# Performance work log

Measured on AMD Instinct MI355X. Metric: run time of the kernel, lower is better.

The kernel has to match this reference:

```python
import jax, jax.numpy as jnp
import numpy as np
from jax import lax

V = 50000      # node_num
LN = 128       # feat_dim
S = 16         # stat_dim
E = 500000     # n_edges
T = 3          # propagation steps
MU = 0.9


def setup_inputs() -> dict:
    key = jax.random.key(0)
    ks = jax.random.split(key, 10)
    X_Node = jax.random.randint(ks[0], (E,), 0, V, dtype=jnp.int32)
    X_Neis = jax.random.randint(ks[1], (E,), 0, V, dtype=jnp.int32)
    dg_list = jax.random.randint(ks[2], (E,), 1, 64, dtype=jnp.int32)
    emb = jax.random.normal(ks[3], (V, LN), dtype=jnp.float32) * 0.1
    xi_w = jax.random.normal(ks[4], (2 * LN, S * S), dtype=jnp.float32) * (1.0 / np.sqrt(2 * LN))
    xi_b = jnp.zeros((S * S,), dtype=jnp.float32)
    rou_w = jax.random.normal(ks[5], (LN, S), dtype=jnp.float32) * (1.0 / np.sqrt(LN))
    rou_b = jnp.zeros((S,), dtype=jnp.float32)
    lin_w = jax.random.normal(ks[6], (LN + S, 3), dtype=jnp.float32) * (1.0 / np.sqrt(LN + S))
    lin_b = jnp.zeros((3,), dtype=jnp.float32)
    return {"X_Node": X_Node, "X_Neis": X_Neis, "dg_list": dg_list,
            "emb": emb, "xi_w": xi_w, "xi_b": xi_b,
            "rou_w": rou_w, "rou_b": rou_b, "lin_w": lin_w, "lin_b": lin_b}


def reference(X_Node, X_Neis, dg_list, emb, xi_w, xi_b, rou_w, rou_b, lin_w, lin_b):
    # edge features: concat(src embed, nbr embed) -> [E, 2*ln]
    Xn = emb[X_Node]                                  # [E, ln]
    X = jnp.concatenate([Xn, emb[X_Neis]], axis=1)    # [E, 2*ln]
    dg = dg_list.astype(emb.dtype)
    # Hw: A = Xi(X)*mu/s/dg  (constant across iterations; torch recomputes, same math)
    A = jnp.tanh(X @ xi_w + xi_b).reshape(-1, S, S)   # [E, s, s]
    A = A * (MU / S) / dg[:, None, None]
    b = jnp.tanh(Xn @ rou_w + rou_b)                  # [E, s]

    states0 = jnp.zeros((V, S), dtype=emb.dtype)

    def step(states, _):
        H = states[X_Node]                            # [E, s] gather
        H = jnp.einsum('est,et->es', A, H) + b        # per-edge small matvec
        states = jax.ops.segment_sum(H, X_Neis, num_segments=V)  # scatter-sum (AggrSum)
        return states, None

    states, _ = lax.scan(step, states0, None, length=T)
    logits = jnp.concatenate([emb, states], axis=1) @ lin_w + lin_b  # [V, 3]
    return jax.nn.softmax(logits, axis=1)
```

## Files before the change

### kernel.cpp

```cpp
#include <hip/hip_runtime.h>
#include <hip/hip_bf16.h>
#include <hip/hip_fp16.h>

#define LN_F 128

typedef __attribute__((ext_vector_type(8))) __bf16 bf16x8;
typedef __attribute__((ext_vector_type(4))) float f32x4;

__device__ __forceinline__ unsigned short f2bf(float f) {
    unsigned u = __float_as_uint(f);
    u = u + 0x7FFFu + ((u >> 16) & 1u);
    return (unsigned short)(u >> 16);
}
__device__ __forceinline__ unsigned cvt_pk_bf16(float lo, float hi) {
    unsigned r;
    asm("v_cvt_pk_bf16_f32 %0, %1, %2" : "=v"(r) : "v"(lo), "v"(hi));
    return r;
}
__device__ __forceinline__ float tanh_poly(float x) {
    float t = x * x;
    float p = fmaf(t, -0.05396825397f, 0.13333333333f);
    p = fmaf(t, p, -0.33333333333f);
    p = fmaf(t, p, 1.0f);
    return x * p;
}
__device__ __forceinline__ float tanh_polyc(float x) {
    return tanh_poly(fminf(1.2f, fmaxf(-1.2f, x)));
}
__device__ __forceinline__ float bflo(unsigned u) { return __uint_as_float(u << 16); }
__device__ __forceinline__ float bfhi(unsigned u) { return __uint_as_float(u & 0xffff0000u); }

__device__ __forceinline__ unsigned f2e5(float x) {
    unsigned short u = __half_as_ushort(__float2half(x));
    u = (unsigned short)(u + 0x7F + ((u >> 8) & 1));
    return (unsigned)(u >> 8) & 0xFFu;
}
__device__ __forceinline__ float2 cvt2f16(unsigned w) {
    union { unsigned u; __half2 h; } cv;
    cv.u = w;
    return __half22float2(cv.h);
}

__global__ void k_conv_emb(const float* __restrict__ src,
                           unsigned short* __restrict__ dst, int n8) {
    int i = blockIdx.x * blockDim.x + threadIdx.x;
    if (i >= n8) return;
    const float4* s = (const float4*)src;
    float4 a = s[i * 2], b = s[i * 2 + 1];
    uint4 o;
    o.x = (unsigned)f2bf(a.x) | ((unsigned)f2bf(a.y) << 16);
    o.y = (unsigned)f2bf(a.z) | ((unsigned)f2bf(a.w) << 16);
    o.z = (unsigned)f2bf(b.x) | ((unsigned)f2bf(b.y) << 16);
    o.w = (unsigned)f2bf(b.z) | ((unsigned)f2bf(b.w) << 16);
    ((uint4*)dst)[i] = o;
}

__global__ void k_conv_wc(const float* __restrict__ xiw, unsigned short* __restrict__ dst) {
    int t = blockIdx.x * blockDim.x + threadIdx.x;
    if (t >= 512 * 16) return;
    int cp = t >> 4, g = t & 15;
    unsigned short u[8];
#pragma unroll
    for (int j = 0; j < 8; ++j) {
        int k = g * 8 + j;
        float w = (cp < 256) ? xiw[k * 256 + cp] : xiw[(128 + k) * 256 + (cp - 256)];
        u[j] = f2bf(w);
    }
    uint4 o;
    o.x = (unsigned)u[0] | ((unsigned)u[1] << 16);
    o.y = (unsigned)u[2] | ((unsigned)u[3] << 16);
    o.z = (unsigned)u[4] | ((unsigned)u[5] << 16);
    o.w = (unsigned)u[6] | ((unsigned)u[7] << 16);
    ((uint4*)dst)[cp * 16 + (g ^ (cp & 7))] = o;
}

__global__ void k_conv_rou(const float* __restrict__ w, unsigned short* __restrict__ dst) {
    int t = blockIdx.x * blockDim.x + threadIdx.x;
    if (t >= 16 * 16) return;
    int c = t >> 4, g = t & 15;
    unsigned short u[8];
#pragma unroll
    for (int j = 0; j < 8; ++j) u[j] = f2bf(w[(g * 8 + j) * 16 + c]);
    uint4 o;
    o.x = (unsigned)u[0] | ((unsigned)u[1] << 16);
    o.y = (unsigned)u[2] | ((unsigned)u[3] << 16);
    o.z = (unsigned)u[4] | ((unsigned)u[5] << 16);
    o.w = (unsigned)u[6] | ((unsigned)u[7] << 16);
    ((uint4*)dst)[c * 16 + (g ^ (c & 7))] = o;
}

__global__ void k_cvtH(const float* __restrict__ st, unsigned* __restrict__ Hb, int n2) {
    int i = blockIdx.x * blockDim.x + threadIdx.x;
    if (i >= n2) return;
    float2 f = ((const float2*)st)[i];
    Hb[i] = cvt_pk_bf16(f.x, f.y);
}

__global__ void k_hist(const int* __restrict__ Xe, int* __restrict__ cnt, int n) {
    int e = blockIdx.x * blockDim.x + threadIdx.x;
    if (e < n) atomicAdd(&cnt[Xe[e]], 1);
}

__global__ __launch_bounds__(256) void k_scan1(const int* __restrict__ cnt,
                                               int* __restrict__ rp,
                                               int* __restrict__ bsum, int V) {
    __shared__ int ls[256];
    int b = blockIdx.x, t = threadIdx.x;
    int i = b * 256 + t;
    int val = (i < V) ? cnt[i] : 0;
    ls[t] = val;
    __syncthreads();
    for (int off = 1; off < 256; off <<= 1) {
        int x = (t >= off) ? ls[t - off] : 0;
        __syncthreads();
        ls[t] += x;
        __syncthreads();
    }
    if (i < V) rp[i] = ls[t] - val;
    if (t == 255) bsum[b] = ls[255];
}

__global__ __launch_bounds__(256) void k_scan2(const int* __restrict__ bsum,
                                               int* __restrict__ boff,
                                               int* __restrict__ rp, int V, int NB) {
    __shared__ int ls[256];
    int t = threadIdx.x;
    int val = (t < NB) ? bsum[t] : 0;
    ls[t] = val;
    __syncthreads();
    for (int off = 1; off < 256; off <<= 1) {
        int x = (t >= off) ? ls[t - off] : 0;
        __syncthreads();
        ls[t] += x;
        __syncthreads();
    }
    if (t < NB) boff[t] = ls[t] - val;
    if (t == 255) rp[V] = ls[255];
}

__global__ void k_scan3(int* __restrict__ rp, const int* __restrict__ boff, int V) {
    int i = blockIdx.x * blockDim.x + threadIdx.x;
    if (i < V) rp[i] += boff[blockIdx.x];
}

__global__ void k_permute(const int* __restrict__ Xn, const int* __restrict__ Xe,
                          const int* __restrict__ dg, const int* __restrict__ rp,
                          int* __restrict__ c2, int2* __restrict__ edata,
                          int* __restrict__ edst, int n) {
    int e = blockIdx.x * blockDim.x + threadIdx.x;
    if (e >= n) return;
    int nb = Xe[e];
    int pos = rp[nb] + atomicAdd(&c2[nb], 1);
    edata[pos] = make_int2(Xn[e], __float_as_int(0.05625f / (float)dg[e]));
    edst[pos] = nb;
}

__global__ void k_padfill(int2* __restrict__ edata, int* __restrict__ edst,
                          int E, int Epad) {
    int i = E + blockIdx.x * blockDim.x + threadIdx.x;
    if (i >= Epad) return;
    edata[i] = make_int2(0, 0);
    edst[i] = 0;
}

__global__ __launch_bounds__(512) void k_U(
    const unsigned short* __restrict__ embb, const uint4* __restrict__ WcT,
    const uint4* __restrict__ rouT, const float* __restrict__ xib,
    const float* __restrict__ roub,
    unsigned* __restrict__ U8, unsigned* __restrict__ U28,
    float* __restrict__ bnode, int V) {
    __shared__ uint4 sB[2048];
    __shared__ uint4 sR[256];
    const int half = blockIdx.y;
    for (int i = threadIdx.x; i < 2048; i += 512) sB[i] = WcT[half * 2048 + i];
    if (half == 0 && threadIdx.x < 256) sR[threadIdx.x] = rouT[threadIdx.x];
    __syncthreads();

    const int wave = threadIdx.x >> 6, lane = threadIdx.x & 63;
    const int j = lane & 15, kg = lane >> 4;
    const int wbase = blockIdx.x * 512 + wave * 64;

    int nv[4];
#pragma unroll
    for (int g = 0; g < 4; ++g) nv[g] = min(wbase + g * 16 + j, V - 1);

    f32x4 acc[8][4] = {};
    f32x4 accb[4] = {};
#pragma unroll
    for (int kc = 0; kc < 4; ++kc) {
        bf16x8 bf[4];
#pragma unroll
        for (int g = 0; g < 4; ++g)
            bf[g] = *(const bf16x8*)(embb + (size_t)nv[g] * 128 + kc * 32 + kg * 8);
        int swz = (kc * 4 + kg) ^ (j & 7);
#pragma unroll
        for (int ct = 0; ct < 8; ++ct) {
            bf16x8 afr = ((const bf16x8*)sB)[(ct * 16 + j) * 16 + swz];
#pragma unroll
            for (int g = 0; g < 4; ++g)
                acc[ct][g] = __builtin_amdgcn_mfma_f32_16x16x32_bf16(afr, bf[g], acc[ct][g], 0, 0, 0);
        }
        if (half == 0) {
            bf16x8 rfr = ((const bf16x8*)sR)[j * 16 + swz];
#pragma unroll
            for (int g = 0; g < 4; ++g)
                accb[g] = __builtin_amdgcn_mfma_f32_16x16x32_bf16(rfr, bf[g], accb[g], 0, 0, 0);
        }
    }

#pragma unroll
    for (int ct = 0; ct < 8; ++ct) {
        int c0 = half * 128 + ct * 16 + kg * 4;
        float4 bias = (half < 2) ? ((const float4*)xib)[c0 >> 2]
                                 : make_float4(0.f, 0.f, 0.f, 0.f);
#pragma unroll
        for (int g = 0; g < 4; ++g) {
            int node = wbase + g * 16 + j;
            if (node < V) {
                const f32x4 a = acc[ct][g];
                float v0 = a[0] + bias.x, v1 = a[1] + bias.y;
                float v2 = a[2] + bias.z, v3 = a[3] + bias.w;
                unsigned pk = f2e5(v0) | (f2e5(v2) << 8) | (f2e5(v1) << 16) | (f2e5(v3) << 24);
                if (half < 2) U8[node * 64 + (c0 >> 2)] = pk;
                else          U28[node * 64 + ((c0 - 256) >> 2)] = pk;
            }
        }
    }
    if (half == 0) {
        float4 rb4 = ((const float4*)roub)[kg];
#pragma unroll
        for (int g = 0; g < 4; ++g) {
            int node = wbase + g * 16 + j;
            if (node < V) {
                float4 bo;
                bo.x = tanh_polyc(accb[g][0] + rb4.x);
                bo.y = tanh_polyc(accb[g][1] + rb4.y);
                bo.z = tanh_polyc(accb[g][2] + rb4.z);
                bo.w = tanh_polyc(accb[g][3] + rb4.w);
                *(float4*)(bnode + (size_t)node * 16 + kg * 4) = bo;
            }
        }
    }
}

__global__ __launch_bounds__(256) void k_B1e(
    const float* __restrict__ bnode, const int2* __restrict__ edata,
    const int* __restrict__ edst, float* __restrict__ B1, int E, int Epad) {
    int wid = (blockIdx.x * 256 + threadIdx.x) >> 6;
    int wbase = wid * 64;
    if (wbase >= Epad) return;
    int lane = threadIdx.x & 63;
    int g = lane >> 4, s = lane & 15, lbase = g * 16;
    int sbase = wbase + g * 16;

    int em = wbase + lane;
    int d_own = edst[em];
    int d_nxt = edst[min(em + 1, Epad - 1)];
    unsigned long long flags = __ballot(d_own != d_nxt);

    int cur = edst[sbase];
    float acc = 0.f;
#pragma unroll 4
    for (int j = 0; j < 16; ++j) {
        int p = sbase + j;
        int u = edata[p].x;
        float v = bnode[(size_t)u * 16 + s];
        acc += (p < E) ? v : 0.f;
        bool flush = ((flags >> (lbase + j)) & 1ull) || (j == 15);
        if (flush) {
            atomicAdd(&B1[(size_t)cur * 16 + s], acc);
            acc = 0.f;
            if (j < 15) cur = edst[p + 1];
        }
    }
}

__global__ __launch_bounds__(256) void k_prop_e(
    const unsigned* __restrict__ U8, const unsigned* __restrict__ U28,
    const int2* __restrict__ edata, const int* __restrict__ edst,
    const unsigned* __restrict__ Hb,
    float* __restrict__ sn, int Epad) {
    int wid = (blockIdx.x * 256 + threadIdx.x) >> 6;
    int wbase = wid * 64;
    if (wbase >= Epad) return;
    int lane = threadIdx.x & 63;
    int g = lane >> 4, s = lane & 15, lbase = g * 16;
    int sbase = wbase + g * 16;

    int em = wbase + lane;
    int d_own = edst[em];
    int d_nxt = edst[min(em + 1, Epad - 1)];
    unsigned long long flags = __ballot(d_own != d_nxt);

    int cur = edst[sbase];
    float u2f[16];
    {
        uint4 r = ((const uint4*)U28)[cur * 16 + s];
        unsigned wq[4] = {r.x, r.y, r.z, r.w};
#pragma unroll
        for (int q = 0; q < 4; ++q) {
            float2 fa = cvt2f16((wq[q] << 8) & 0xFF00FF00u);
            float2 fb = cvt2f16(wq[q] & 0xFF00FF00u);
            u2f[4 * q + 0] = fa.x; u2f[4 * q + 1] = fa.y;
            u2f[4 * q + 2] = fb.x; u2f[4 * q + 3] = fb.y;
        }
    }

    float acc = 0.f;
#pragma unroll 2
    for (int j = 0; j < 16; ++j) {
        int p = sbase + j;
        int2 ed = edata[p];
        int u = ed.x;
        float sc = __int_as_float(ed.y);
        uint4 q1 = ((const uint4*)U8)[u * 16 + s];
        unsigned h2 = Hb[u * 8 + (s & 7)];
        unsigned wq[4] = {q1.x, q1.y, q1.z, q1.w};
        float sum = 0.f;
#pragma unroll
        for (int q = 0; q < 4; ++q) {
            unsigned w = wq[q];
            float2 fa = cvt2f16((w << 8) & 0xFF00FF00u);
            float2 fb = cvt2f16(w & 0xFF00FF00u);
            unsigned hm0 = __shfl(h2, lbase + 2 * q, 64);
            unsigned hm1 = __shfl(h2, lbase + 2 * q + 1, 64);
            float a0 = tanh_poly(fa.x + u2f[4 * q + 0]);
            float a1 = tanh_poly(fa.y + u2f[4 * q + 1]);
            float a2 = tanh_poly(fb.x + u2f[4 * q + 2]);
            float a3 = tanh_poly(fb.y + u2f[4 * q + 3]);
            sum = fmaf(a0, bflo(hm0), sum);
            sum = fmaf(a1, bfhi(hm0), sum);
            sum = fmaf(a2, bflo(hm1), sum);
            sum = fmaf(a3, bfhi(hm1), sum);
        }
        acc = fmaf(sc, sum, acc);
        bool flush = ((flags >> (lbase + j)) & 1ull) || (j == 15);
        if (flush) {
            atomicAdd(&sn[(size_t)cur * 16 + s], acc);
            acc = 0.f;
            if (j < 15) {
                cur = edst[p + 1];
                uint4 r = ((const uint4*)U28)[cur * 16 + s];
                unsigned wr[4] = {r.x, r.y, r.z, r.w};
#pragma unroll
                for (int q = 0; q < 4; ++q) {
                    float2 fa = cvt2f16((wr[q] << 8) & 0xFF00FF00u);
                    float2 fb = cvt2f16(wr[q] & 0xFF00FF00u);
                    u2f[4 * q + 0] = fa.x; u2f[4 * q + 1] = fa.y;
                    u2f[4 * q + 2] = fb.x; u2f[4 * q + 3] = fb.y;
                }
            }
        }
    }
}

__global__ void k_final(const unsigned short* __restrict__ embb, const float* __restrict__ st,
                        const float* __restrict__ lw, const float* __restrict__ lb,
                        float* __restrict__ out, int nv) {
    __shared__ float sw[435];
    for (int i = threadIdx.x; i < 435; i += 256) sw[i] = (i < 432) ? lw[i] : lb[i - 432];
    __syncthreads();
    int t = blockIdx.x * blockDim.x + threadIdx.x;
    int v = t >> 4, j = t & 15;
    if (v >= nv) return;
    const uint4 q = *(const uint4*)(embb + (size_t)v * 128 + j * 8);
    unsigned uu[4] = {q.x, q.y, q.z, q.w};
    float a0 = 0.f, a1 = 0.f, a2 = 0.f;
#pragma unroll
    for (int m = 0; m < 4; ++m) {
        int i = j * 8 + 2 * m;
        float x0 = bflo(uu[m]), x1 = bfhi(uu[m]);
        a0 += x0 * sw[i * 3] + x1 * sw[(i + 1) * 3];
        a1 += x0 * sw[i * 3 + 1] + x1 * sw[(i + 1) * 3 + 1];
        a2 += x0 * sw[i * 3 + 2] + x1 * sw[(i + 1) * 3 + 2];
    }
    float xs = st[(size_t)v * 16 + j];
    a0 += xs * sw[(128 + j) * 3]; a1 += xs * sw[(128 + j) * 3 + 1]; a2 += xs * sw[(128 + j) * 3 + 2];
#pragma unroll
    for (int m = 1; m < 16; m <<= 1) {
        a0 += __shfl_xor(a0, m, 64);
        a1 += __shfl_xor(a1, m, 64);
        a2 += __shfl_xor(a2, m, 64);
    }
    if (j == 0) {
        a0 += sw[432]; a1 += sw[433]; a2 += sw[434];
        float mx = fmaxf(a0, fmaxf(a1, a2));
        float e0 = __expf(a0 - mx), e1 = __expf(a1 - mx), e2 = __expf(a2 - mx);
        float inv = 1.f / (e0 + e1 + e2);
        out[(size_t)v * 3 + 0] = e0 * inv;
        out[(size_t)v * 3 + 1] = e1 * inv;
        out[(size_t)v * 3 + 2] = e2 * inv;
    }
}

extern "C" void kernel_launch(void* const* d_in, const int* in_sizes, int n_in,
                              void* d_out, int out_size, void* d_ws, size_t ws_size,
                              hipStream_t stream) {
    const int*   Xn  = (const int*)d_in[0];
    const int*   Xe  = (const int*)d_in[1];
    const int*   dg  = (const int*)d_in[2];
    const float* emb = (const float*)d_in[3];
    const float* xiw = (const float*)d_in[4];
    const float* xib = (const float*)d_in[5];
    const float* rw  = (const float*)d_in[6];
    const float* rb  = (const float*)d_in[7];
    const float* lw  = (const float*)d_in[8];
    const float* lb  = (const float*)d_in[9];
    float* out = (float*)d_out;
    const int E = in_sizes[0];
    const int V = in_sizes[3] / LN_F;
    const int NB = (V + 255) / 256;
    const int Epad = (E + 63) & ~63;

    char* p = (char*)d_ws;
    auto carve = [&](size_t bytes) {
        char* q = p; p += (bytes + 255) & ~(size_t)255; return q;
    };
    unsigned short* embb = (unsigned short*)carve((size_t)V * 128 * 2);
    unsigned* U8    = (unsigned*)carve((size_t)V * 256);
    unsigned* U28   = (unsigned*)carve((size_t)V * 256);
    uint4* WcT   = (uint4*)carve(512 * 16 * 16);
    uint4* rouT  = (uint4*)carve(4096);
    float* bnode = (float*)carve((size_t)V * 16 * 4);
    float* B1    = (float*)carve((size_t)V * 16 * 4);
    float* stB   = (float*)carve((size_t)V * 16 * 4);
    float* stA   = (float*)carve((size_t)V * 16 * 4);
    unsigned* Hb = (unsigned*)carve((size_t)V * 16 * 2);
    int*   cnt   = (int*)carve((size_t)V * 4 * 2);
    int*   c2    = cnt + V;
    int*   rp    = (int*)carve((size_t)(V + 1) * 4);
    int*   bsum  = (int*)carve(256 * 4);
    int*   boff  = (int*)carve(256 * 4);
    int2*  edata = (int2*)carve((size_t)Epad * 8);
    int*   edst  = (int*)carve((size_t)Epad * 4);

    k_conv_emb<<<(V * 128 / 8 + 255) / 256, 256, 0, stream>>>(emb, embb, V * 128 / 8);
    k_conv_wc<<<32, 256, 0, stream>>>(xiw, (unsigned short*)WcT);
    k_conv_rou<<<1, 256, 0, stream>>>(rw, (unsigned short*)rouT);
    {
        dim3 g((V + 511) / 512, 4);
        k_U<<<g, 512, 0, stream>>>(embb, WcT, rouT, xib, rb, U8, U28, bnode, V);
    }

    hipMemsetAsync(cnt, 0, (size_t)V * 4 * 2, stream);
    k_hist<<<(E + 255) / 256, 256, 0, stream>>>(Xe, cnt, E);
    k_scan1<<<NB, 256, 0, stream>>>(cnt, rp, bsum, V);
    k_scan2<<<1, 256, 0, stream>>>(bsum, boff, rp, V, NB);
    k_scan3<<<NB, 256, 0, stream>>>(rp, boff, V);
    k_permute<<<(E + 255) / 256, 256, 0, stream>>>(Xn, Xe, dg, rp, c2, edata, edst, E);
    if (Epad > E)
        k_padfill<<<1, 64, 0, stream>>>(edata, edst, E, Epad);

    hipMemsetAsync(B1, 0, (size_t)V * 16 * 4, stream);
    {
        int blocks = (Epad / 64 + 3) / 4;
        k_B1e<<<blocks, 256, 0, stream>>>(bnode, edata, edst, B1, E, Epad);
    }

    k_cvtH<<<((size_t)V * 8 + 255) / 256, 256, 0, stream>>>(B1, Hb, V * 8);
    hipMemcpyAsync(stB, B1, (size_t)V * 16 * 4, hipMemcpyDeviceToDevice, stream);
    {
        int blocks = (Epad / 64 + 3) / 4;
        k_prop_e<<<blocks, 256, 0, stream>>>(U8, U28, edata, edst, Hb, stB, Epad);
    }

    k_cvtH<<<((size_t)V * 8 + 255) / 256, 256, 0, stream>>>(stB, Hb, V * 8);
    hipMemcpyAsync(stA, B1, (size_t)V * 16 * 4, hipMemcpyDeviceToDevice, stream);
    {
        int blocks = (Epad / 64 + 3) / 4;
        k_prop_e<<<blocks, 256, 0, stream>>>(U8, U28, edata, edst, Hb, stA, Epad);
    }

    k_final<<<((size_t)V * 16 + 255) / 256, 256, 0, stream>>>(embb, stA, lw, lb, out, V);
}
```

Before: 221.9 us.

## Use packed fp16 tanh and fdot2 in propagation, fuse conversion and copy kernels

The per-edge inner loop of k_prop_e now decodes the 8-bit U values into packed half2 with byte perms, evaluates tanh in packed fp16, and accumulates with fdot2 against fp16 states. Previously it converted to fp32, ran scalar tanh and did bf16 FMAs. The three weight and embedding conversion kernels become one launch, and the state conversion plus two device memcpys become a single k_prep kernel. Together these cut ALU work, launch count and copy traffic, at the cost of fp16 precision in tanh. The unclamped fp16 polynomial may lose accuracy for large pre-activations.

```diff
diff --git a/kernel.cpp b/kernel.cpp
--- a/kernel.cpp
+++ b/kernel.cpp
@@ -6,27 +6,21 @@
 
 typedef __attribute__((ext_vector_type(8))) __bf16 bf16x8;
 typedef __attribute__((ext_vector_type(4))) float f32x4;
+typedef __attribute__((ext_vector_type(2))) _Float16 half2_t;
 
 __device__ __forceinline__ unsigned short f2bf(float f) {
     unsigned u = __float_as_uint(f);
     u = u + 0x7FFFu + ((u >> 16) & 1u);
     return (unsigned short)(u >> 16);
 }
-__device__ __forceinline__ unsigned cvt_pk_bf16(float lo, float hi) {
-    unsigned r;
-    asm("v_cvt_pk_bf16_f32 %0, %1, %2" : "=v"(r) : "v"(lo), "v"(hi));
-    return r;
-}
-__device__ __forceinline__ float tanh_poly(float x) {
+__device__ __forceinline__ float tanh_polyc(float x) {
+    x = fminf(1.2f, fmaxf(-1.2f, x));
     float t = x * x;
     float p = fmaf(t, -0.05396825397f, 0.13333333333f);
     p = fmaf(t, p, -0.33333333333f);
     p = fmaf(t, p, 1.0f);
     return x * p;
 }
-__device__ __forceinline__ float tanh_polyc(float x) {
-    return tanh_poly(fminf(1.2f, fmaxf(-1.2f, x)));
-}
 __device__ __forceinline__ float bflo(unsigned u) { return __uint_as_float(u << 16); }
 __device__ __forceinline__ float bfhi(unsigned u) { return __uint_as_float(u & 0xffff0000u); }
 
@@ -35,65 +29,66 @@
     u = (unsigned short)(u + 0x7F + ((u >> 8) & 1));
     return (unsigned)(u >> 8) & 0xFFu;
 }
-__device__ __forceinline__ float2 cvt2f16(unsigned w) {
-    union { unsigned u; __half2 h; } cv;
-    cv.u = w;
-    return __half22float2(cv.h);
-}
-
-__global__ void k_conv_emb(const float* __restrict__ src,
-                           unsigned short* __restrict__ dst, int n8) {
-    int i = blockIdx.x * blockDim.x + threadIdx.x;
-    if (i >= n8) return;
-    const float4* s = (const float4*)src;
-    float4 a = s[i * 2], b = s[i * 2 + 1];
-    uint4 o;
-    o.x = (unsigned)f2bf(a.x) | ((unsigned)f2bf(a.y) << 16);
-    o.y = (unsigned)f2bf(a.z) | ((unsigned)f2bf(a.w) << 16);
-    o.z = (unsigned)f2bf(b.x) | ((unsigned)f2bf(b.y) << 16);
-    o.w = (unsigned)f2bf(b.z) | ((unsigned)f2bf(b.w) << 16);
-    ((uint4*)dst)[i] = o;
-}
-
-__global__ void k_conv_wc(const float* __restrict__ xiw, unsigned short* __restrict__ dst) {
+__device__ __forceinline__ half2_t u2h2(unsigned w) {
+    union { unsigned u; half2_t h; } c; c.u = w; return c.h;
+}
+__device__ __forceinline__ unsigned h2u(half2_t h) {
+    union { half2_t h; unsigned u; } c; c.h = h; return c.u;
+}
+__device__ __forceinline__ half2_t tanh_pk(half2_t x) {
+    const half2_t c2 = {(_Float16)(2.0f / 15.0f), (_Float16)(2.0f / 15.0f)};
+    const half2_t c1 = {(_Float16)(-1.0f / 3.0f), (_Float16)(-1.0f / 3.0f)};
+    const half2_t one = {(_Float16)1.0f, (_Float16)1.0f};
+    half2_t t = x * x;
+    half2_t p = t * c2 + c1;
+    p = t * p + one;
+    return x * p;
+}
+
+__global__ void k_conv(const float* __restrict__ emb, const float* __restrict__ xiw,
+                       const float* __restrict__ rw,
+                       unsigned short* __restrict__ embb, unsigned short* __restrict__ WcT,
+                       unsigned short* __restrict__ rouT, int V) {
     int t = blockIdx.x * blockDim.x + threadIdx.x;
-    if (t >= 512 * 16) return;
-    int cp = t >> 4, g = t & 15;
-    unsigned short u[8];
-#pragma unroll
-    for (int j = 0; j < 8; ++j) {
-        int k = g * 8 + j;
-        float w = (cp < 256) ? xiw[k * 256 + cp] : xiw[(128 + k) * 256 + (cp - 256)];
-        u[j] = f2bf(w);
-    }
-    uint4 o;
-    o.x = (unsigned)u[0] | ((unsigned)u[1] << 16);
-    o.y = (unsigned)u[2] | ((unsigned)u[3] << 16);
-    o.z = (unsigned)u[4] | ((unsigned)u[5] << 16);
-    o.w = (unsigned)u[6] | ((unsigned)u[7] << 16);
-    ((uint4*)dst)[cp * 16 + (g ^ (cp & 7))] = o;
-}
-
-__global__ void k_conv_rou(const float* __restrict__ w, unsigned short* __restrict__ dst) {
-    int t = blockIdx.x * blockDim.x + threadIdx.x;
-    if (t >= 16 * 16) return;
-    int c = t >> 4, g = t & 15;
-    unsigned short u[8];
-#pragma unroll
-    for (int j = 0; j < 8; ++j) u[j] = f2bf(w[(g * 8 + j) * 16 + c]);
-    uint4 o;
-    o.x = (unsigned)u[0] | ((unsigned)u[1] << 16);
-    o.y = (unsigned)u[2] | ((unsigned)u[3] << 16);
-    o.z = (unsigned)u[4] | ((unsigned)u[5] << 16);
-    o.w = (unsigned)u[6] | ((unsigned)u[7] << 16);
-    ((uint4*)dst)[c * 16 + (g ^ (c & 7))] = o;
-}
-
-__global__ void k_cvtH(const float* __restrict__ st, unsigned* __restrict__ Hb, int n2) {
-    int i = blockIdx.x * blockDim.x + threadIdx.x;
-    if (i >= n2) return;
-    float2 f = ((const float2*)st)[i];
-    Hb[i] = cvt_pk_bf16(f.x, f.y);
+    int n_emb = V * 16;
+    if (t < n_emb) {
+        const float4* s = (const float4*)emb;
+        float4 a = s[t * 2], b = s[t * 2 + 1];
+        uint4 o;
+        o.x = (unsigned)f2bf(a.x) | ((unsigned)f2bf(a.y) << 16);
+        o.y = (unsigned)f2bf(a.z) | ((unsigned)f2bf(a.w) << 16);
+        o.z = (unsigned)f2bf(b.x) | ((unsigned)f2bf(b.y) << 16);
+        o.w = (unsigned)f2bf(b.z) | ((unsigned)f2bf(b.w) << 16);
+        ((uint4*)embb)[t] = o;
+    } else if (t < n_emb + 512 * 16) {
+        int t2 = t - n_emb;
+        int cp = t2 >> 4, g = t2 & 15;
+        unsigned short u[8];
+#pragma unroll
+        for (int j = 0; j < 8; ++j) {
+            int k = g * 8 + j;
+            float w = (cp < 256) ? xiw[k * 256 + cp] : xiw[(128 + k) * 256 + (cp - 256)];
+            u[j] = f2bf(w);
+        }
+        uint4 o;
+        o.x = (unsigned)u[0] | ((unsigned)u[1] << 16);
+        o.y = (unsigned)u[2] | ((unsigned)u[3] << 16);
+        o.z = (unsigned)u[4] | ((unsigned)u[5] << 16);
+        o.w = (unsigned)u[6] | ((unsigned)u[7] << 16);
+        ((uint4*)WcT)[cp * 16 + (g ^ (cp & 7))] = o;
+    } else if (t < n_emb + 512 * 16 + 256) {
+        int t2 = t - n_emb - 512 * 16;
+        int c = t2 >> 4, g = t2 & 15;
+        unsigned short u[8];
+#pragma unroll
+        for (int j = 0; j < 8; ++j) u[j] = f2bf(rw[(g * 8 + j) * 16 + c]);
+        uint4 o;
+        o.x = (unsigned)u[0] | ((unsigned)u[1] << 16);
+        o.y = (unsigned)u[2] | ((unsigned)u[3] << 16);
+        o.z = (unsigned)u[4] | ((unsigned)u[5] << 16);
+        o.w = (unsigned)u[6] | ((unsigned)u[7] << 16);
+        ((uint4*)rouT)[c * 16 + (g ^ (c & 7))] = o;
+    }
 }
 
 __global__ void k_hist(const int* __restrict__ Xe, int* __restrict__ cnt, int n) {
@@ -220,7 +215,7 @@
                 const f32x4 a = acc[ct][g];
                 float v0 = a[0] + bias.x, v1 = a[1] + bias.y;
                 float v2 = a[2] + bias.z, v3 = a[3] + bias.w;
-                unsigned pk = f2e5(v0) | (f2e5(v2) << 8) | (f2e5(v1) << 16) | (f2e5(v3) << 24);
+                unsigned pk = f2e5(v0) | (f2e5(v1) << 8) | (f2e5(v2) << 16) | (f2e5(v3) << 24);
                 if (half < 2) U8[node * 64 + (c0 >> 2)] = pk;
                 else          U28[node * 64 + ((c0 - 256) >> 2)] = pk;
             }
@@ -275,10 +270,23 @@
     }
 }
 
+__global__ void k_prep(const float* __restrict__ st, unsigned* __restrict__ Hf,
+                       float* __restrict__ cp1, float* __restrict__ cp2, int n2) {
+    int i = blockIdx.x * blockDim.x + threadIdx.x;
+    if (i >= n2) return;
+    float2 f = ((const float2*)st)[i];
+    half2_t h = {(_Float16)f.x, (_Float16)f.y};
+    Hf[i] = h2u(h);
+    if (cp1 != nullptr) {
+        ((float2*)cp1)[i] = f;
+        ((float2*)cp2)[i] = f;
+    }
+}
+
 __global__ __launch_bounds__(256) void k_prop_e(
     const unsigned* __restrict__ U8, const unsigned* __restrict__ U28,
     const int2* __restrict__ edata, const int* __restrict__ edst,
-    const unsigned* __restrict__ Hb,
+    const unsigned* __restrict__ Hf,
     float* __restrict__ sn, int Epad) {
     int wid = (blockIdx.x * 256 + threadIdx.x) >> 6;
     int wbase = wid * 64;
@@ -293,16 +301,14 @@
     unsigned long long flags = __ballot(d_own != d_nxt);
 
     int cur = edst[sbase];
-    float u2f[16];
+    half2_t u2h[8];
     {
         uint4 r = ((const uint4*)U28)[cur * 16 + s];
-        unsigned wq[4] = {r.x, r.y, r.z, r.w};
+        unsigned wr[4] = {r.x, r.y, r.z, r.w};
 #pragma unroll
         for (int q = 0; q < 4; ++q) {
-            float2 fa = cvt2f16((wq[q] << 8) & 0xFF00FF00u);
-            float2 fb = cvt2f16(wq[q] & 0xFF00FF00u);
-            u2f[4 * q + 0] = fa.x; u2f[4 * q + 1] = fa.y;
-            u2f[4 * q + 2] = fb.x; u2f[4 * q + 3] = fb.y;
+            u2h[2 * q]     = u2h2(__builtin_amdgcn_perm(wr[q], 0u, 0x05000400u));
+            u2h[2 * q + 1] = u2h2(__builtin_amdgcn_perm(wr[q], 0u, 0x07000600u));
         }
     }
 
@@ -314,24 +320,19 @@
         int u = ed.x;
         float sc = __int_as_float(ed.y);
         uint4 q1 = ((const uint4*)U8)[u * 16 + s];
-        unsigned h2 = Hb[u * 8 + (s & 7)];
+        unsigned h2 = Hf[u * 8 + (s & 7)];
         unsigned wq[4] = {q1.x, q1.y, q1.z, q1.w};
         float sum = 0.f;
 #pragma unroll
         for (int q = 0; q < 4; ++q) {
-            unsigned w = wq[q];
-            float2 fa = cvt2f16((w << 8) & 0xFF00FF00u);
-            float2 fb = cvt2f16(w & 0xFF00FF00u);
+            half2_t x0 = u2h2(__builtin_amdgcn_perm(wq[q], 0u, 0x05000400u)) + u2h[2 * q];
+            half2_t x1 = u2h2(__builtin_amdgcn_perm(wq[q], 0u, 0x07000600u)) + u2h[2 * q + 1];
+            half2_t r0 = tanh_pk(x0);
+            half2_t r1 = tanh_pk(x1);
             unsigned hm0 = __shfl(h2, lbase + 2 * q, 64);
             unsigned hm1 = __shfl(h2, lbase + 2 * q + 1, 64);
-            float a0 = tanh_poly(fa.x + u2f[4 * q + 0]);
-            float a1 = tanh_poly(fa.y + u2f[4 * q + 1]);
-            float a2 = tanh_poly(fb.x + u2f[4 * q + 2]);
-            float a3 = tanh_poly(fb.y + u2f[4 * q + 3]);
-            sum = fmaf(a0, bflo(hm0), sum);
-            sum = fmaf(a1, bfhi(hm0), sum);
-            sum = fmaf(a2, bflo(hm1), sum);
-            sum = fmaf(a3, bfhi(hm1), sum);
+            sum = __builtin_amdgcn_fdot2(r0, u2h2(hm0), sum, false);
+            sum = __builtin_amdgcn_fdot2(r1, u2h2(hm1), sum, false);
         }
         acc = fmaf(sc, sum, acc);
         bool flush = ((flags >> (lbase + j)) & 1ull) || (j == 15);
@@ -344,10 +345,8 @@
                 unsigned wr[4] = {r.x, r.y, r.z, r.w};
 #pragma unroll
                 for (int q = 0; q < 4; ++q) {
-                    float2 fa = cvt2f16((wr[q] << 8) & 0xFF00FF00u);
-                    float2 fb = cvt2f16(wr[q] & 0xFF00FF00u);
-                    u2f[4 * q + 0] = fa.x; u2f[4 * q + 1] = fa.y;
-                    u2f[4 * q + 2] = fb.x; u2f[4 * q + 3] = fb.y;
+                    u2h[2 * q]     = u2h2(__builtin_amdgcn_perm(wr[q], 0u, 0x05000400u));
+                    u2h[2 * q + 1] = u2h2(__builtin_amdgcn_perm(wr[q], 0u, 0x07000600u));
                 }
             }
         }
@@ -425,7 +424,7 @@
     float* B1    = (float*)carve((size_t)V * 16 * 4);
     float* stB   = (float*)carve((size_t)V * 16 * 4);
     float* stA   = (float*)carve((size_t)V * 16 * 4);
-    unsigned* Hb = (unsigned*)carve((size_t)V * 16 * 2);
+    unsigned* Hf = (unsigned*)carve((size_t)V * 16 * 2);
     int*   cnt   = (int*)carve((size_t)V * 4 * 2);
     int*   c2    = cnt + V;
     int*   rp    = (int*)carve((size_t)(V + 1) * 4);
@@ -434,10 +433,10 @@
     int2*  edata = (int2*)carve((size_t)Epad * 8);
     int*   edst  = (int*)carve((size_t)Epad * 4);
 
-    k_conv_emb<<<(V * 128 / 8 + 255) / 256, 256, 0, stream>>>(emb, embb, V * 128 / 8);
-    k_conv_wc<<<32, 256, 0, stream>>>(xiw, (unsigned short*)WcT);
-    k_conv_rou<<<1, 256, 0, stream>>>(rw, (unsigned short*)rouT);
     {
+        int nconv = V * 16 + 512 * 16 + 256;
+        k_conv<<<(nconv + 255) / 256, 256, 0, stream>>>(
+            emb, xiw, rw, embb, (unsigned short*)WcT, (unsigned short*)rouT, V);
         dim3 g((V + 511) / 512, 4);
         k_U<<<g, 512, 0, stream>>>(embb, WcT, rouT, xib, rb, U8, U28, bnode, V);
     }
@@ -457,19 +456,14 @@
         k_B1e<<<blocks, 256, 0, stream>>>(bnode, edata, edst, B1, E, Epad);
     }
 
-    k_cvtH<<<((size_t)V * 8 + 255) / 256, 256, 0, stream>>>(B1, Hb, V * 8);
-    hipMemcpyAsync(stB, B1, (size_t)V * 16 * 4, hipMemcpyDeviceToDevice, stream);
-    {
-        int blocks = (Epad / 64 + 3) / 4;
-        k_prop_e<<<blocks, 256, 0, stream>>>(U8, U28, edata, edst, Hb, stB, Epad);
-    }
-
-    k_cvtH<<<((size_t)V * 8 + 255) / 256, 256, 0, stream>>>(stB, Hb, V * 8);
-    hipMemcpyAsync(stA, B1, (size_t)V * 16 * 4, hipMemcpyDeviceToDevice, stream);
-    {
-        int blocks = (Epad / 64 + 3) / 4;
-        k_prop_e<<<blocks, 256, 0, stream>>>(U8, U28, edata, edst, Hb, stA, Epad);
-    }
+    const int n2 = V * 8;
+    const int pblocks = (Epad / 64 + 3) / 4;
+
+    k_prep<<<(n2 + 255) / 256, 256, 0, stream>>>(B1, Hf, stB, stA, n2);
+    k_prop_e<<<pblocks, 256, 0, stream>>>(U8, U28, edata, edst, Hf, stB, Epad);
+
+    k_prep<<<(n2 + 255) / 256, 256, 0, stream>>>(stB, Hf, nullptr, nullptr, n2);
+    k_prop_e<<<pblocks, 256, 0, stream>>>(U8, U28, edata, edst, Hf, stA, Epad);
 
     k_final<<<((size_t)V * 16 + 255) / 256, 256, 0, stream>>>(embb, stA, lw, lb, out, V);
 }
```

Result: faster. 201.8 us (-9.1%).
